# Performance work log

Measured on AMD Instinct MI355X. Metric: run time of the kernel, lower is better.

Reference implementation:

```python
import jax, jax.numpy as jnp
import numpy as np

N = 30000   # total nodes
E = 240000  # edges
B = 64      # graphs / proteins
H = 10      # GATv2 heads
C = 78      # per-head out dim (= xd_features)
D = H * C   # 780
SEQ = 1000
EMB = 128
LH = 64     # LSTM hidden per direction


def _lstm_dir(xs, Wih, Whh, bih, bhh, reverse):
    # xs: [T, Bn, EMB]; PyTorch gate order i,f,g,o
    Bn = xs.shape[1]
    h0 = jnp.zeros((Bn, LH), xs.dtype)
    def step(carry, xt):
        h, c = carry
        z = xt @ Wih.T + h @ Whh.T + bih + bhh
        i, f, g, o = jnp.split(z, 4, axis=-1)
        c = jax.nn.sigmoid(f) * c + jax.nn.sigmoid(i) * jnp.tanh(g)
        h = jax.nn.sigmoid(o) * jnp.tanh(c)
        return (h, c), h
    _, hs = jax.lax.scan(step, (h0, h0), xs, reverse=reverse)
    return hs


def setup_inputs() -> dict:
    k = jax.random.key(0)
    nxt = lambda i: jax.random.fold_in(k, i)
    s = 0.05
    d = {}
    d['x'] = jax.random.normal(nxt(0), (N, C), jnp.float32)
    d['edge_index'] = jax.random.randint(nxt(1), (2, E), 0, N)
    d['batch'] = jnp.sort(jax.random.randint(nxt(2), (N,), 0, B))
    d['target'] = jax.random.randint(nxt(3), (B, SEQ), 0, 26)
    # GATv2Conv params (share_weights=False)
    d['Wl'] = jax.random.normal(nxt(4), (C, D), jnp.float32) * s
    d['Wr'] = jax.random.normal(nxt(5), (C, D), jnp.float32) * s
    d['att'] = jax.random.normal(nxt(6), (H, C), jnp.float32) * s
    d['gat_b'] = jnp.zeros((D,), jnp.float32)
    # GCNConv params
    d['gcn_w'] = jax.random.normal(nxt(7), (D, D), jnp.float32) * s
    d['gcn_b'] = jnp.zeros((D,), jnp.float32)
    # protein branch
    d['emb'] = jax.random.normal(nxt(8), (26, EMB), jnp.float32) * s
    for tag, base in (('f', 9), ('b', 13)):
        d['Wih_' + tag] = jax.random.normal(nxt(base), (4 * LH, EMB), jnp.float32) * s
        d['Whh_' + tag] = jax.random.normal(nxt(base + 1), (4 * LH, LH), jnp.float32) * s
        d['bih_' + tag] = jnp.zeros((4 * LH,), jnp.float32)
        d['bhh_' + tag] = jnp.zeros((4 * LH,), jnp.float32)
    d['conv_w'] = jax.random.normal(nxt(17), (32, SEQ, 8), jnp.float32) * s
    d['conv_b'] = jnp.zeros((32,), jnp.float32)
    d['fcp_w'] = jax.random.normal(nxt(18), (32 * 121, 128), jnp.float32) * s
    d['fcp_b'] = jnp.zeros((128,), jnp.float32)
    # combined MLP (actual concat dim = 2*780 + 128 = 1688)
    d['fc1_w'] = jax.random.normal(nxt(19), (1688, 1024), jnp.float32) * s
    d['fc1_b'] = jnp.zeros((1024,), jnp.float32)
    d['fc2_w'] = jax.random.normal(nxt(20), (1024, 512), jnp.float32) * s
    d['fc2_b'] = jnp.zeros((512,), jnp.float32)
    d['out_w'] = jax.random.normal(nxt(21), (512, 1), jnp.float32) * s
    d['out_b'] = jnp.zeros((1,), jnp.float32)
    return d


def reference(x, edge_index, batch, target, Wl, Wr, att, gat_b, gcn_w, gcn_b,
              emb, Wih_f, Whh_f, bih_f, bhh_f, Wih_b, Whh_b, bih_b, bhh_b,
              conv_w, conv_b, fcp_w, fcp_b, fc1_w, fc1_b, fc2_w, fc2_b,
              out_w, out_b):
    # ---- graph branch (eval mode: dropout off) ----
    loops = jnp.arange(N)
    src = jnp.concatenate([edge_index[0], loops])  # self loops (PyG default)
    dst = jnp.concatenate([edge_index[1], loops])

    # GATv2Conv
    xl = (x @ Wl).reshape(N, H, C)
    xr = (x @ Wr).reshape(N, H, C)
    e = jax.nn.leaky_relu(xl[src] + xr[dst], 0.2)       # [E+N, H, C]
    logit = jnp.einsum('ehc,hc->eh', e, att)            # [E+N, H]
    m = jax.ops.segment_max(logit, dst, num_segments=N)
    ex = jnp.exp(logit - m[dst])
    den = jax.ops.segment_sum(ex, dst, num_segments=N)
    alpha = ex / den[dst]
    h = jax.ops.segment_sum(alpha[:, :, None] * xl[src], dst, num_segments=N)
    h = jax.nn.elu(h.reshape(N, D) + gat_b)

    # GCNConv with symmetric normalization
    hw = h @ gcn_w
    deg = jax.ops.segment_sum(jnp.ones_like(src, jnp.float32), dst, num_segments=N)
    dinv = jnp.where(deg > 0, jax.lax.rsqrt(jnp.maximum(deg, 1e-12)), 0.0)
    norm = dinv[src] * dinv[dst]
    g = jax.ops.segment_sum(norm[:, None] * hw[src], dst, num_segments=N) + gcn_b
    g = jax.nn.relu(g)

    # global max + mean pooling per graph
    gmax = jax.ops.segment_max(g, batch, num_segments=B)
    cnt = jax.ops.segment_sum(jnp.ones((N,), jnp.float32), batch, num_segments=B)
    gmean = jax.ops.segment_sum(g, batch, num_segments=B) / jnp.maximum(cnt, 1.0)[:, None]
    graph_feat = jnp.concatenate([gmax, gmean], axis=1)  # [B, 1560]

    # ---- protein branch ----
    et = emb[target]                                     # [B, SEQ, EMB]
    # nn.LSTM default batch_first=False: time axis is axis 0 (=B), batch axis is SEQ
    hf = _lstm_dir(et, Wih_f, Whh_f, bih_f, bhh_f, reverse=False)
    hb = _lstm_dir(et, Wih_b, Whh_b, bih_b, bhh_b, reverse=True)
    hcat = jnp.concatenate([hf, hb], axis=-1)            # [B, SEQ, 128]
    conv = jax.lax.conv_general_dilated(hcat, conv_w, (1,), 'VALID',
                                        dimension_numbers=('NCH', 'OIH', 'NCH'))
    conv = conv + conv_b[None, :, None]                  # [B, 32, 121]
    prot = conv.reshape(B, 32 * 121) @ fcp_w + fcp_b     # [B, 128]

    # ---- combined head ----
    comb = jnp.concatenate([graph_feat, prot], axis=1)   # [B, 1688]
    h1 = jax.nn.relu(comb @ fc1_w + fc1_b)
    h2 = jax.nn.relu(h1 @ fc2_w + fc2_b)
    return h2 @ out_w + out_b                            # [B, 1]
```

## Files before the change

kernel.cpp:

```cpp
#include <hip/hip_runtime.h>
#include <hip/hip_bf16.h>
#include <math.h>

static constexpr int NN   = 30000;
static constexpr int EE   = 240000;
static constexpr int ET   = EE + NN;
static constexpr int BB   = 64;
static constexpr int HH   = 10;
static constexpr int CC   = 78;
static constexpr int CCP  = 80;
static constexpr int DD   = HH * CC;
static constexpr int DDP  = HH * CCP;
static constexpr int NNP  = 30080;
static constexpr int KXP  = 96;
static constexpr int NBP  = 896;
static constexpr int SEQ  = 1000;
static constexpr int EMB  = 128;
static constexpr int LH   = 64;
static constexpr int COMBD = 2 * DD + 128;
static constexpr int PCHUNK = 64;

typedef __attribute__((ext_vector_type(8))) short short8;
typedef __attribute__((ext_vector_type(4))) float f32x4;

__device__ __forceinline__ float bf2f(unsigned short u) {
    return __uint_as_float(((unsigned int)u) << 16);
}
__device__ __forceinline__ float bflo(unsigned int u) {
    return __uint_as_float(u << 16);
}
__device__ __forceinline__ float bfhi(unsigned int u) {
    return __uint_as_float(u & 0xffff0000u);
}
__device__ __forceinline__ unsigned int pack2bf(float x, float y) {
    __hip_bfloat16 bx = __float2bfloat16(x), by = __float2bfloat16(y);
    unsigned short ux = *reinterpret_cast<unsigned short*>(&bx);
    unsigned short uy = *reinterpret_cast<unsigned short*>(&by);
    return (unsigned int)ux | ((unsigned int)uy << 16);
}
__device__ __forceinline__ float fast_sigmoid(float x) {
    return __builtin_amdgcn_rcpf(1.f + __expf(-x));
}
__device__ __forceinline__ float fast_tanh(float x) {
    float e = __expf(2.f * x);
    return 1.f - 2.f * __builtin_amdgcn_rcpf(e + 1.f);
}
__device__ __forceinline__ void glds16(const unsigned short* g, unsigned short* l) {
    __builtin_amdgcn_global_load_lds(
        (const __attribute__((address_space(1))) unsigned int*)g,
        (__attribute__((address_space(3))) unsigned int*)l, 16, 0, 0);
}

template <int PADHEAD>
__global__ __launch_bounds__(256) void gemm_glds(const __hip_bfloat16* __restrict__ A,
                                                 const __hip_bfloat16* __restrict__ Bt,
                                                 __hip_bfloat16* __restrict__ C,
                                                 int M, int N, int Kp, int ldc) {
    __shared__ unsigned short As[128 * 32];
    __shared__ unsigned short Bs[128 * 32];
    const int tid  = threadIdx.x;
    const int lane = tid & 63, wid = tid >> 6;
    const int wr = wid >> 1, wc = wid & 1;
    const int l15 = lane & 15, l4 = lane >> 4;
    int l = blockIdx.y * gridDim.x + blockIdx.x;
    {
        int nwg = gridDim.x * gridDim.y;
        int q = nwg >> 3, r = nwg & 7;
        int xcd = l & 7, idx = l >> 3;
        l = (xcd < r) ? (xcd * (q + 1) + idx) : (r * (q + 1) + (xcd - r) * q + idx);
    }
    const int bm = (l / gridDim.x) * 128;
    const int bn = (l % gridDim.x) * 128;
    const unsigned short* Au = (const unsigned short*)A;
    const unsigned short* Bu = (const unsigned short*)Bt;
    const int lrow = lane >> 2, lseg = (lane & 3) * 8;

    f32x4 acc[4][4];
#pragma unroll
    for (int m = 0; m < 4; ++m)
#pragma unroll
        for (int n = 0; n < 4; ++n) acc[m][n] = (f32x4){0.f, 0.f, 0.f, 0.f};

    for (int k0 = 0; k0 < Kp; k0 += 32) {
#pragma unroll
        for (int c = 0; c < 2; ++c) {
            int rbase = wid * 32 + c * 16;
            glds16(Au + (size_t)(bm + rbase + lrow) * Kp + k0 + lseg, &As[rbase * 32]);
            glds16(Bu + (size_t)(bn + rbase + lrow) * Kp + k0 + lseg, &Bs[rbase * 32]);
        }
        __syncthreads();
        short8 a[4], b[4];
#pragma unroll
        for (int m = 0; m < 4; ++m)
            a[m] = *reinterpret_cast<const short8*>(&As[(wr * 64 + m * 16 + l15) * 32 + l4 * 8]);
#pragma unroll
        for (int n = 0; n < 4; ++n)
            b[n] = *reinterpret_cast<const short8*>(&Bs[(wc * 64 + n * 16 + l15) * 32 + l4 * 8]);
#pragma unroll
        for (int m = 0; m < 4; ++m)
#pragma unroll
            for (int n = 0; n < 4; ++n)
                acc[m][n] = __builtin_amdgcn_mfma_f32_16x16x32_bf16(a[m], b[n], acc[m][n], 0, 0, 0);
        __syncthreads();
    }
#pragma unroll
    for (int m = 0; m < 4; ++m)
#pragma unroll
        for (int n = 0; n < 4; ++n)
#pragma unroll
            for (int r = 0; r < 4; ++r) {
                int row = bm + wr * 64 + m * 16 + l4 * 4 + r;
                int col = bn + wc * 64 + n * 16 + l15;
                if (row < M && col < N) {
                    int pc = PADHEAD ? ((col / CC) * CCP + (col % CC)) : col;
                    C[(size_t)row * ldc + pc] = __float2bfloat16(acc[m][n][r]);
                }
            }
}

template <int OBF, int PADHEAD>
__global__ __launch_bounds__(256) void gemm_bf16_mfma(const __hip_bfloat16* __restrict__ A,
                                                      const __hip_bfloat16* __restrict__ Bt,
                                                      void* __restrict__ Cv,
                                                      int M, int N, int K, int ldc) {
    constexpr int LDS_S = 40;
    __shared__ unsigned short As[128 * LDS_S];
    __shared__ unsigned short Bs[128 * LDS_S];
    const int tid  = threadIdx.x;
    const int lane = tid & 63, wid = tid >> 6;
    const int wr = wid >> 1, wc = wid & 1;
    const int l15 = lane & 15, l4 = lane >> 4;
    int l = blockIdx.y * gridDim.x + blockIdx.x;
    {
        int nwg = gridDim.x * gridDim.y;
        int q = nwg >> 3, r = nwg & 7;
        int xcd = l & 7, idx = l >> 3;
        l = (xcd < r) ? (xcd * (q + 1) + idx) : (r * (q + 1) + (xcd - r) * q + idx);
    }
    const int bm = (l / gridDim.x) * 128;
    const int bn = (l % gridDim.x) * 128;
    const int tr = tid >> 2, tc = (tid & 3) * 8;

    const unsigned short* Au = (const unsigned short*)A;
    const unsigned short* Bu = (const unsigned short*)Bt;

    f32x4 acc[4][4];
#pragma unroll
    for (int m = 0; m < 4; ++m)
#pragma unroll
        for (int n = 0; n < 4; ++n) acc[m][n] = (f32x4){0.f, 0.f, 0.f, 0.f};

    for (int k0 = 0; k0 < K; k0 += 32) {
#pragma unroll
        for (int half = 0; half < 2; ++half) {
            int row = tr + half * 64;
            {
                int grow = bm + row;
                short8 sv;
                if (grow < M && k0 + tc + 8 <= K) {
                    const unsigned int* p = (const unsigned int*)(Au + (size_t)grow * K + k0 + tc);
#pragma unroll
                    for (int j = 0; j < 4; ++j) {
                        unsigned int u = p[j];
                        sv[2 * j]     = (short)(u & 0xffffu);
                        sv[2 * j + 1] = (short)(u >> 16);
                    }
                } else {
#pragma unroll
                    for (int j = 0; j < 8; ++j) {
                        int gk = k0 + tc + j;
                        sv[j] = (grow < M && gk < K) ? (short)Au[(size_t)grow * K + gk] : (short)0;
                    }
                }
                *reinterpret_cast<short8*>(&As[row * LDS_S + tc]) = sv;
            }
            {
                int grow = bn + row;
                short8 sv;
                if (grow < N && k0 + tc + 8 <= K) {
                    const unsigned int* p = (const unsigned int*)(Bu + (size_t)grow * K + k0 + tc);
#pragma unroll
                    for (int j = 0; j < 4; ++j) {
                        unsigned int u = p[j];
                        sv[2 * j]     = (short)(u & 0xffffu);
                        sv[2 * j + 1] = (short)(u >> 16);
                    }
                } else {
#pragma unroll
                    for (int j = 0; j < 8; ++j) {
                        int gk = k0 + tc + j;
                        sv[j] = (grow < N && gk < K) ? (short)Bu[(size_t)grow * K + gk] : (short)0;
                    }
                }
                *reinterpret_cast<short8*>(&Bs[row * LDS_S + tc]) = sv;
            }
        }
        __syncthreads();
        short8 a[4], b[4];
#pragma unroll
        for (int m = 0; m < 4; ++m)
            a[m] = *reinterpret_cast<const short8*>(&As[(wr * 64 + m * 16 + l15) * LDS_S + l4 * 8]);
#pragma unroll
        for (int n = 0; n < 4; ++n)
            b[n] = *reinterpret_cast<const short8*>(&Bs[(wc * 64 + n * 16 + l15) * LDS_S + l4 * 8]);
#pragma unroll
        for (int m = 0; m < 4; ++m)
#pragma unroll
            for (int n = 0; n < 4; ++n)
                acc[m][n] = __builtin_amdgcn_mfma_f32_16x16x32_bf16(a[m], b[n], acc[m][n], 0, 0, 0);
        __syncthreads();
    }
#pragma unroll
    for (int m = 0; m < 4; ++m)
#pragma unroll
        for (int n = 0; n < 4; ++n)
#pragma unroll
            for (int r = 0; r < 4; ++r) {
                int row = bm + wr * 64 + m * 16 + l4 * 4 + r;
                int col = bn + wc * 64 + n * 16 + l15;
                if (row < M && col < N) {
                    int pc = PADHEAD ? ((col / CC) * CCP + (col % CC)) : col;
                    if (OBF)
                        ((__hip_bfloat16*)Cv)[(size_t)row * ldc + pc] = __float2bfloat16(acc[m][n][r]);
                    else
                        ((float*)Cv)[(size_t)row * ldc + pc] = acc[m][n][r];
                }
            }
}

__global__ void pad_x(const float* __restrict__ x, __hip_bfloat16* __restrict__ xp) {
    int idx = blockIdx.x * blockDim.x + threadIdx.x;
    if (idx >= NNP * KXP) return;
    int r = idx / KXP, c = idx % KXP;
    float v = (r < NN && c < CC) ? x[(size_t)r * CC + c] : 0.f;
    xp[idx] = __float2bfloat16(v);
}

__global__ void pad_wT(const float* __restrict__ w, __hip_bfloat16* __restrict__ wt) {
    int idx = blockIdx.x * blockDim.x + threadIdx.x;
    if (idx >= NBP * KXP) return;
    int n = idx / KXP, k = idx % KXP;
    float v = (n < DD && k < CC) ? w[(size_t)k * DD + n] : 0.f;
    wt[idx] = __float2bfloat16(v);
}

__global__ void pad_gcwT(const float* __restrict__ w, __hip_bfloat16* __restrict__ wt) {
    int idx = blockIdx.x * blockDim.x + threadIdx.x;
    if (idx >= NBP * DDP) return;
    int n = idx / DDP, kp = idx % DDP;
    int kc = kp % CCP;
    int k = (kp / CCP) * CC + kc;
    float v = (n < DD && kc < CC) ? w[(size_t)k * DD + n] : 0.f;
    wt[idx] = __float2bfloat16(v);
}

__global__ void transpose_f32(const float* __restrict__ in, float* __restrict__ out,
                              int Kdim, int Ndim) {
    int idx = blockIdx.x * blockDim.x + threadIdx.x;
    if (idx >= Kdim * Ndim) return;
    int n = idx / Kdim, k = idx % Kdim;
    out[idx] = in[(size_t)k * Ndim + n];
}

__global__ void pad_att(const float* __restrict__ att, float* __restrict__ att_p) {
    int idx = blockIdx.x * blockDim.x + threadIdx.x;
    if (idx >= HH * CCP) return;
    int h = idx / CCP, c = idx % CCP;
    att_p[idx] = (c < CC) ? att[h * CC + c] : 0.f;
}

__global__ void zero_pads(unsigned int* __restrict__ a, unsigned int* __restrict__ b) {
    int idx = blockIdx.x * blockDim.x + threadIdx.x;
    if (idx >= NN * HH) return;
    int n = idx / HH, h = idx % HH;
    size_t p = ((size_t)n * DDP + h * CCP + CC) >> 1;
    a[p] = 0u;
    b[p] = 0u;
}

template <int ACT>
__global__ __launch_bounds__(256) void gemm_skinny(const float* __restrict__ A,
                                                   const float* __restrict__ Bt,
                                                   const float* __restrict__ bias,
                                                   float* __restrict__ C,
                                                   int M, int N, int K, int ldc) {
    int oidx = blockIdx.x * 4 + (threadIdx.x >> 6);
    int lane = threadIdx.x & 63;
    if (oidx >= M * N) return;
    int row = oidx / N, col = oidx % N;
    const float4* a = (const float4*)(A + (size_t)row * K);
    const float4* b = (const float4*)(Bt + (size_t)col * K);
    int K4 = K >> 2;
    float s = 0.f;
    for (int i = lane; i < K4; i += 64) {
        float4 x = a[i], y = b[i];
        s += x.x * y.x + x.y * y.y + x.z * y.z + x.w * y.w;
    }
#pragma unroll
    for (int off = 32; off; off >>= 1) s += __shfl_xor(s, off);
    if (lane == 0) {
        s += bias[col];
        if (ACT == 1) s = fmaxf(s, 0.f);
        C[(size_t)row * ldc + col] = s;
    }
}

__global__ void deg_count(const int* __restrict__ ei, int* __restrict__ deg) {
    int e = blockIdx.x * blockDim.x + threadIdx.x;
    if (e >= ET) return;
    int d = (e < EE) ? ei[EE + e] : (e - EE);
    atomicAdd(&deg[d], 1);
}

__global__ __launch_bounds__(1024) void scan_kernel(const int* __restrict__ deg,
                                                    int* __restrict__ offs) {
    __shared__ int lds[1024];
    int tid = threadIdx.x;
    const int chunk = (NN + 1023) / 1024;
    int base = tid * chunk;
    int s = 0;
    for (int i = 0; i < chunk; ++i) {
        int idx = base + i;
        if (idx < NN) s += deg[idx];
    }
    lds[tid] = s;
    __syncthreads();
    for (int d = 1; d < 1024; d <<= 1) {
        int v = (tid >= d) ? lds[tid - d] : 0;
        __syncthreads();
        lds[tid] += v;
        __syncthreads();
    }
    int run = (tid == 0) ? 0 : lds[tid - 1];
    for (int i = 0; i < chunk; ++i) {
        int idx = base + i;
        if (idx < NN) { offs[idx] = run; run += deg[idx]; }
    }
    if (tid == 1023) offs[NN] = lds[1023];
}

__global__ void csr_fill(const int* __restrict__ ei, const int* __restrict__ offs,
                         int* __restrict__ cursor, int* __restrict__ csr_src,
                         int* __restrict__ csr_dst) {
    int e = blockIdx.x * blockDim.x + threadIdx.x;
    if (e >= ET) return;
    int s = (e < EE) ? ei[e] : (e - EE);
    int d = (e < EE) ? ei[EE + e] : (e - EE);
    int pos = atomicAdd(&cursor[d], 1);
    int slot = offs[d] + pos;
    csr_src[slot] = s;
    csr_dst[slot] = d;
}

__global__ void dinv_kernel(const int* __restrict__ deg, float* __restrict__ dinv) {
    int n = blockIdx.x * blockDim.x + threadIdx.x;
    if (n >= NN) return;
    float dg = (float)deg[n];
    dinv[n] = (dg > 0.f) ? 1.f / sqrtf(dg) : 0.f;
}

__device__ __forceinline__ float dot2lr(unsigned int a, unsigned int b, float w0, float w1) {
    float v0 = bflo(a) + bflo(b);
    float v1 = bfhi(a) + bfhi(b);
    v0 = (v0 > 0.f) ? v0 : 0.2f * v0;
    v1 = (v1 > 0.f) ? v1 : 0.2f * v1;
    return w0 * v0 + w1 * v1;
}

__global__ void gat_logits(const unsigned short* __restrict__ xl,
                           const unsigned short* __restrict__ xr,
                           const float* __restrict__ att_p, const int* __restrict__ csr_src,
                           const int* __restrict__ csr_dst, float* __restrict__ logit) {
    int idx = blockIdx.x * blockDim.x + threadIdx.x;
    if (idx >= ET * HH) return;
    int i = idx / HH, h = idx % HH;
    int s = csr_src[i], d = csr_dst[i];
    const uint4* pl = (const uint4*)(xl + (size_t)s * DDP + h * CCP);
    const uint4* pr = (const uint4*)(xr + (size_t)d * DDP + h * CCP);
    const float* pa = att_p + h * CCP;
    float acc = 0.f;
#pragma unroll
    for (int q = 0; q < CCP / 8; ++q) {
        uint4 a = pl[q], b = pr[q];
        const float* p8 = pa + q * 8;
        acc += dot2lr(a.x, b.x, p8[0], p8[1]);
        acc += dot2lr(a.y, b.y, p8[2], p8[3]);
        acc += dot2lr(a.z, b.z, p8[4], p8[5]);
        acc += dot2lr(a.w, b.w, p8[6], p8[7]);
    }
    logit[idx] = acc;
}

__global__ void gat_softmax(const int* __restrict__ offs, float* __restrict__ logit) {
    int idx = blockIdx.x * blockDim.x + threadIdx.x;
    if (idx >= NN * HH) return;
    int n = idx / HH, h = idx % HH;
    int i0 = offs[n], i1 = offs[n + 1];
    float m = -1e30f;
    for (int i = i0; i < i1; ++i) m = fmaxf(m, logit[i * HH + h]);
    float den = 0.f;
    for (int i = i0; i < i1; ++i) {
        float e = __expf(logit[i * HH + h] - m);
        logit[i * HH + h] = e;
        den += e;
    }
    float inv = __builtin_amdgcn_rcpf(den);
    for (int i = i0; i < i1; ++i) logit[i * HH + h] *= inv;
}

__global__ __launch_bounds__(256) void gat_aggregate(const int* __restrict__ offs,
                                                     const int* __restrict__ csr_src,
                                                     const float* __restrict__ alpha,
                                                     const unsigned int* __restrict__ xl,
                                                     const float* __restrict__ gat_b,
                                                     unsigned int* __restrict__ hout) {
    int n = blockIdx.x;
    int tid = threadIdx.x;
    int i0 = offs[n], i1 = offs[n + 1];
    const int U = DDP / 2;
    int u0 = tid, u1 = tid + 256;
    bool v1 = (u1 < U);
    int h0 = u0 / (CCP / 2), h1 = v1 ? u1 / (CCP / 2) : 0;
    float lo0 = 0.f, hi0 = 0.f, lo1 = 0.f, hi1 = 0.f;
    for (int i = i0; i < i1; ++i) {
        const unsigned int* row = xl + (size_t)csr_src[i] * U;
        const float* al = alpha + (size_t)i * HH;
        unsigned int w0 = row[u0];
        float p0 = al[h0];
        lo0 += p0 * bflo(w0);
        hi0 += p0 * bfhi(w0);
        if (v1) {
            unsigned int w1 = row[u1];
            float p1 = al[h1];
            lo1 += p1 * bflo(w1);
            hi1 += p1 * bfhi(w1);
        }
    }
    unsigned int ov0 = 0u, ov1 = 0u;
    int m0 = u0 % (CCP / 2);
    if (m0 != (CCP / 2 - 1)) {
        int d = h0 * CC + 2 * m0;
        float x = lo0 + gat_b[d];     x = (x > 0.f) ? x : __expf(x) - 1.f;
        float y = hi0 + gat_b[d + 1]; y = (y > 0.f) ? y : __expf(y) - 1.f;
        ov0 = pack2bf(x, y);
    }
    hout[(size_t)n * U + u0] = ov0;
    if (v1) {
        int m1 = u1 % (CCP / 2);
        if (m1 != (CCP / 2 - 1)) {
            int d = h1 * CC + 2 * m1;
            float x = lo1 + gat_b[d];     x = (x > 0.f) ? x : __expf(x) - 1.f;
            float y = hi1 + gat_b[d + 1]; y = (y > 0.f) ? y : __expf(y) - 1.f;
            ov1 = pack2bf(x, y);
        }
        hout[(size_t)n * U + u1] = ov1;
    }
}

__global__ __launch_bounds__(256) void gcn_aggregate(const int* __restrict__ offs,
                                                     const int* __restrict__ csr_src,
                                                     const float* __restrict__ dinv,
                                                     const unsigned int* __restrict__ hw,
                                                     const float* __restrict__ gcn_b,
                                                     unsigned int* __restrict__ g) {
    int n = blockIdx.x;
    int tid = threadIdx.x;
    float din = dinv[n];
    int i0 = offs[n], i1 = offs[n + 1];
    const int U = DDP / 2;
    int u0 = tid, u1 = tid + 256;
    bool v1 = (u1 < U);
    float lo0 = 0.f, hi0 = 0.f, lo1 = 0.f, hi1 = 0.f;
    for (int i = i0; i < i1; ++i) {
        int s = csr_src[i];
        float w = dinv[s] * din;
        const unsigned int* row = hw + (size_t)s * U;
        unsigned int w0 = row[u0];
        lo0 += w * bflo(w0);
        hi0 += w * bfhi(w0);
        if (v1) {
            unsigned int w1 = row[u1];
            lo1 += w * bflo(w1);
            hi1 += w * bfhi(w1);
        }
    }
    int m0 = u0 % (CCP / 2);
    if (m0 != (CCP / 2 - 1)) {
        int d = (u0 / (CCP / 2)) * CC + 2 * m0;
        float x = fmaxf(lo0 + gcn_b[d], 0.f);
        float y = fmaxf(hi0 + gcn_b[d + 1], 0.f);
        g[(size_t)n * U + u0] = pack2bf(x, y);
    }
    if (v1) {
        int m1 = u1 % (CCP / 2);
        if (m1 != (CCP / 2 - 1)) {
            int d = (u1 / (CCP / 2)) * CC + 2 * m1;
            float x = fmaxf(lo1 + gcn_b[d], 0.f);
            float y = fmaxf(hi1 + gcn_b[d + 1], 0.f);
            g[(size_t)n * U + u1] = pack2bf(x, y);
        }
    }
}

__global__ void graph_ranges(const int* __restrict__ batch, int* __restrict__ gstart,
                             int* __restrict__ gend) {
    int n = blockIdx.x * blockDim.x + threadIdx.x;
    if (n >= NN) return;
    int b = batch[n];
    if (n == 0 || batch[n - 1] != b) gstart[b] = n;
    if (n == NN - 1 || batch[n + 1] != b) gend[b] = n + 1;
}

__global__ __launch_bounds__(256) void pool_partial(const unsigned int* __restrict__ g,
                                                    const int* __restrict__ batch,
                                                    float* __restrict__ pmax,
                                                    float* __restrict__ psum) {
    int chunk0 = blockIdx.x * PCHUNK;
    int tid = threadIdx.x;
    __shared__ int bsh[PCHUNK];
    for (int i = tid; i < PCHUNK; i += 256) {
        int n = chunk0 + i;
        bsh[i] = (n < NN) ? batch[n] : -1;
    }
    __syncthreads();
    const int U = DDP / 2;
    int u0 = tid, u1 = tid + 256;
    bool v1 = (u1 < U);
    float mA = 0.f, mB = 0.f, mC = 0.f, mD = 0.f;
    float sA = 0.f, sB = 0.f, sC = 0.f, sD = 0.f;
    int curb = bsh[0];
    auto flush = [&](int b) {
        if (b >= 0) {
            int m0 = u0 % (CCP / 2);
            if (m0 != (CCP / 2 - 1)) {
                int d = (u0 / (CCP / 2)) * CC + 2 * m0;
                atomicMax((unsigned int*)&pmax[(size_t)b * DD + d], __float_as_uint(mA));
                atomicAdd(&psum[(size_t)b * DD + d], sA);
                atomicMax((unsigned int*)&pmax[(size_t)b * DD + d + 1], __float_as_uint(mB));
                atomicAdd(&psum[(size_t)b * DD + d + 1], sB);
            }
            if (v1) {
                int m1 = u1 % (CCP / 2);
                if (m1 != (CCP / 2 - 1)) {
                    int d = (u1 / (CCP / 2)) * CC + 2 * m1;
                    atomicMax((unsigned int*)&pmax[(size_t)b * DD + d], __float_as_uint(mC));
                    atomicAdd(&psum[(size_t)b * DD + d], sC);
                    atomicMax((unsigned int*)&pmax[(size_t)b * DD + d + 1], __float_as_uint(mD));
                    atomicAdd(&psum[(size_t)b * DD + d + 1], sD);
                }
            }
        }
        mA = mB = mC = mD = 0.f;
        sA = sB = sC = sD = 0.f;
    };
    for (int i = 0; i < PCHUNK; ++i) {
        int n = chunk0 + i;
        if (n >= NN) break;
        int b = bsh[i];
        if (b != curb) { flush(curb); curb = b; }
        const unsigned int* row = g + (size_t)n * U;
        unsigned int w0 = row[u0];
        float x = bflo(w0), y = bfhi(w0);
        mA = fmaxf(mA, x); sA += x;
        mB = fmaxf(mB, y); sB += y;
        if (v1) {
            unsigned int w1 = row[u1];
            float z = bflo(w1), t = bfhi(w1);
            mC = fmaxf(mC, z); sC += z;
            mD = fmaxf(mD, t); sD += t;
        }
    }
    flush(curb);
}

__global__ void pool_finalize(const float* __restrict__ pmax, const float* __restrict__ psum,
                              const int* __restrict__ gstart, const int* __restrict__ gend,
                              float* __restrict__ comb) {
    int idx = blockIdx.x * blockDim.x + threadIdx.x;
    if (idx >= BB * DD) return;
    int b = idx / DD, d = idx % DD;
    float cnt = fmaxf((float)(gend[b] - gstart[b]), 1.f);
    comb[(size_t)b * COMBD + d] = pmax[idx];
    comb[(size_t)b * COMBD + DD + d] = psum[idx] / cnt;
}

__global__ void proj26_kernel(const float* __restrict__ emb,
                              const float* __restrict__ Wih_f, const float* __restrict__ bih_f,
                              const float* __restrict__ bhh_f,
                              const float* __restrict__ Wih_b, const float* __restrict__ bih_b,
                              const float* __restrict__ bhh_b, float* __restrict__ proj) {
    int dir = blockIdx.x, row = blockIdx.y, j = threadIdx.x;
    const float* W = dir ? Wih_b : Wih_f;
    const float* b1 = dir ? bih_b : bih_f;
    const float* b2 = dir ? bhh_b : bhh_f;
    float acc = b1[j] + b2[j];
    const float* e = emb + row * EMB;
    const float* w = W + j * EMB;
    for (int k = 0; k < EMB; ++k) acc += e[k] * w[k];
    proj[(dir * 26 + row) * 256 + j] = acc;
}

__global__ __launch_bounds__(256) void lstm_kernel(const int* __restrict__ target,
                                                   const float* __restrict__ proj26,
                                                   const float* __restrict__ Whh_f,
                                                   const float* __restrict__ Whh_b,
                                                   float* __restrict__ hcat) {
    int n = blockIdx.x;
    int dir = blockIdx.y;
    int tid = threadIdx.x;
    const float* Whh = dir ? Whh_b : Whh_f;
    const float* proj = proj26 + dir * 26 * 256;
    const int gate = tid >> 6;
    float w[LH];
#pragma unroll
    for (int u4 = 0; u4 < LH / 4; ++u4) {
        float4 v = *reinterpret_cast<const float4*>(Whh + tid * LH + u4 * 4);
        w[u4 * 4 + 0] = v.x; w[u4 * 4 + 1] = v.y;
        w[u4 * 4 + 2] = v.z; w[u4 * 4 + 3] = v.w;
    }
    __shared__ float h_lds[LH];
    __shared__ float z_lds[256];
    float c_reg = 0.f;
    if (tid < LH) h_lds[tid] = 0.f;
    __syncthreads();
    for (int s = 0; s < BB; ++s) {
        int t = dir ? (BB - 1 - s) : s;
        int tgt = target[t * SEQ + n];
        float a0 = 0.f, a1 = 0.f, a2 = 0.f, a3 = 0.f;
#pragma unroll
        for (int u = 0; u < LH; u += 4) {
            a0 += w[u] * h_lds[u];
            a1 += w[u + 1] * h_lds[u + 1];
            a2 += w[u + 2] * h_lds[u + 2];
            a3 += w[u + 3] * h_lds[u + 3];
        }
        float z = proj[tgt * 256 + tid] + a0 + a1 + a2 + a3;
        z_lds[tid] = (gate == 2) ? fast_tanh(z) : fast_sigmoid(z);
        __syncthreads();
        if (tid < LH) {
            float ig = z_lds[tid];
            float fg = z_lds[LH + tid];
            float gg = z_lds[2 * LH + tid];
            float og = z_lds[3 * LH + tid];
            float c = fg * c_reg + ig * gg;
            float h = og * fast_tanh(c);
            c_reg = c;
            h_lds[tid] = h;
            hcat[((size_t)t * SEQ + n) * 128 + dir * LH + tid] = h;
        }
        __syncthreads();
    }
}

__global__ __launch_bounds__(256) void transpose_hcat(const float* __restrict__ hcat,
                                                      unsigned short* __restrict__ hcatT) {
    int b = blockIdx.z;
    int i0 = blockIdx.y * 32;
    int h0 = blockIdx.x * 32;
    int th = threadIdx.x & 31;
    int ti = threadIdx.x >> 5;
    __shared__ float t[32][33];
#pragma unroll
    for (int r = 0; r < 4; ++r) {
        int i = i0 + ti + r * 8;
        if (i < SEQ) t[ti + r * 8][th] = hcat[((size_t)b * SEQ + i) * 128 + h0 + th];
    }
    __syncthreads();
#pragma unroll
    for (int r = 0; r < 4; ++r) {
        int h = h0 + ti + r * 8;
        int i = i0 + th;
        if (i < SEQ) {
            unsigned int u = __float_as_uint(t[th][ti + r * 8]);
            unsigned int lsb = (u >> 16) & 1u;
            u += 0x7fffu + lsb;
            hcatT[((size_t)b * 128 + h) * SEQ + i] = (unsigned short)(u >> 16);
        }
    }
}

__global__ void reshape_convw(const float* __restrict__ conv_w, __hip_bfloat16* __restrict__ wT) {
    int idx = blockIdx.x * blockDim.x + threadIdx.x;
    if (idx >= 256 * SEQ) return;
    int np = idx / SEQ, i = idx % SEQ;
    int o = np >> 3, k = np & 7;
    wT[idx] = __float2bfloat16(conv_w[((size_t)o * SEQ + i) * 8 + k]);
}

__global__ void conv_finalize(const float* __restrict__ T, const float* __restrict__ conv_b,
                              float* __restrict__ convout) {
    int idx = blockIdx.x * blockDim.x + threadIdx.x;
    if (idx >= BB * 32 * 121) return;
    int p = idx % 121;
    int o = (idx / 121) % 32;
    int b = idx / (121 * 32);
    float acc = conv_b[o];
#pragma unroll
    for (int k = 0; k < 8; ++k)
        acc += T[(size_t)(b * 128 + p + k) * 256 + o * 8 + k];
    convout[(size_t)b * 3872 + o * 121 + p] = acc;
}

extern "C" void kernel_launch(void* const* d_in, const int* in_sizes, int n_in,
                              void* d_out, int out_size, void* d_ws, size_t ws_size,
                              hipStream_t stream) {
    const float* x      = (const float*)d_in[0];
    const int*   ei     = (const int*)d_in[1];
    const int*   batch  = (const int*)d_in[2];
    const int*   target = (const int*)d_in[3];
    const float* Wl     = (const float*)d_in[4];
    const float* Wr     = (const float*)d_in[5];
    const float* att    = (const float*)d_in[6];
    const float* gat_b  = (const float*)d_in[7];
    const float* gcn_w  = (const float*)d_in[8];
    const float* gcn_b  = (const float*)d_in[9];
    const float* emb    = (const float*)d_in[10];
    const float* Wih_f  = (const float*)d_in[11];
    const float* Whh_f  = (const float*)d_in[12];
    const float* bih_f  = (const float*)d_in[13];
    const float* bhh_f  = (const float*)d_in[14];
    const float* Wih_b  = (const float*)d_in[15];
    const float* Whh_b  = (const float*)d_in[16];
    const float* bih_b  = (const float*)d_in[17];
    const float* bhh_b  = (const float*)d_in[18];
    const float* conv_w = (const float*)d_in[19];
    const float* conv_b = (const float*)d_in[20];
    const float* fcp_w  = (const float*)d_in[21];
    const float* fcp_b  = (const float*)d_in[22];
    const float* fc1_w  = (const float*)d_in[23];
    const float* fc1_b  = (const float*)d_in[24];
    const float* fc2_w  = (const float*)d_in[25];
    const float* fc2_b  = (const float*)d_in[26];
    const float* out_w  = (const float*)d_in[27];
    const float* out_b  = (const float*)d_in[28];
    float* out = (float*)d_out;
    (void)n_in; (void)in_sizes; (void)out_size;

    char* ws = (char*)d_ws;
    size_t o = 0;
    auto alloc = [&](size_t bytes) {
        char* p = ws + o;
        o = (o + bytes + 255) & ~(size_t)255;
        return p;
    };
    constexpr size_t HALF = (size_t)NN * DDP * 2;
    char* region = (char*)alloc(2 * HALF);
    __hip_bfloat16* xl_bf = (__hip_bfloat16*)region;
    __hip_bfloat16* xr_bf = (__hip_bfloat16*)(region + HALF);
    __hip_bfloat16* hw_bf = (__hip_bfloat16*)region;
    __hip_bfloat16* g_bf  = (__hip_bfloat16*)(region + HALF);
    char* rp = region;
    auto palloc = [&](size_t bytes) {
        char* p = rp;
        rp += (bytes + 255) & ~(size_t)255;
        return p;
    };
    float* hcat    = (float*)palloc((size_t)BB * SEQ * 128 * 4);
    float* proj26  = (float*)palloc(2 * 26 * 256 * 4);
    float* convout = (float*)palloc((size_t)BB * 3872 * 4);
    __hip_bfloat16* wT = (__hip_bfloat16*)palloc((size_t)256 * SEQ * 2);
    unsigned short* hcatT = (unsigned short*)palloc((size_t)BB * 128 * SEQ * 2);
    float* T = (float*)palloc((size_t)BB * 128 * 256 * 4);
    __hip_bfloat16* h_bf  = (__hip_bfloat16*)alloc((size_t)NNP * DDP * 2);
    __hip_bfloat16* x_bf  = (__hip_bfloat16*)alloc((size_t)NNP * KXP * 2);
    __hip_bfloat16* wl_t  = (__hip_bfloat16*)alloc((size_t)NBP * KXP * 2);
    __hip_bfloat16* wr_t  = (__hip_bfloat16*)alloc((size_t)NBP * KXP * 2);
    __hip_bfloat16* gcw_t = (__hip_bfloat16*)alloc((size_t)NBP * DDP * 2);
    float* att_p  = (float*)alloc((size_t)HH * CCP * 4);
    float* fcp_wt = (float*)alloc((size_t)3872 * 128 * 4);
    float* fc1_wt = (float*)alloc((size_t)COMBD * 1024 * 4);
    float* fc2_wt = (float*)alloc((size_t)1024 * 512 * 4);
    float* out_wt = (float*)alloc((size_t)512 * 4);
    float* logit    = (float*)alloc((size_t)ET * HH * 4);
    int*   csr_src  = (int*)alloc((size_t)ET * 4);
    int*   csr_dst  = (int*)alloc((size_t)ET * 4);
    int*   deg      = (int*)alloc((size_t)NN * 4);
    int*   cursor   = (int*)alloc((size_t)NN * 4);
    int*   offs     = (int*)alloc((size_t)(NN + 1) * 4);
    float* dinv     = (float*)alloc((size_t)NN * 4);
    int*   gstart   = (int*)alloc(64 * 4);
    int*   gend     = (int*)alloc(64 * 4);
    float* pmax     = (float*)alloc((size_t)BB * DD * 4);
    float* psum     = (float*)alloc((size_t)BB * DD * 4);
    float* comb     = (float*)alloc((size_t)BB * COMBD * 4);
    float* h1       = (float*)alloc((size_t)BB * 1024 * 4);
    float* h2       = (float*)alloc((size_t)BB * 512 * 4);
    if (o > ws_size) return;

    hipMemsetAsync(deg, 0, (size_t)NN * 4, stream);
    hipMemsetAsync(cursor, 0, (size_t)NN * 4, stream);
    hipMemsetAsync(gstart, 0, 64 * 4, stream);
    hipMemsetAsync(gend, 0, 64 * 4, stream);
    hipMemsetAsync(pmax, 0, (size_t)BB * DD * 4, stream);
    hipMemsetAsync(psum, 0, (size_t)BB * DD * 4, stream);

    {
        dim3 grid(2, 26);
        proj26_kernel<<<grid, 256, 0, stream>>>(emb, Wih_f, bih_f, bhh_f, Wih_b, bih_b, bhh_b, proj26);
    }
    {
        dim3 grid(SEQ, 2);
        lstm_kernel<<<grid, 256, 0, stream>>>(target, proj26, Whh_f, Whh_b, hcat);
    }
    {
        dim3 grid(4, 32, BB);
        transpose_hcat<<<grid, 256, 0, stream>>>(hcat, hcatT);
    }
    reshape_convw<<<(256 * SEQ + 255) / 256, 256, 0, stream>>>(conv_w, wT);
    {
        dim3 grid(2, 64);
        gemm_bf16_mfma<0, 0><<<grid, 256, 0, stream>>>((const __hip_bfloat16*)hcatT, wT, T,
                                                       BB * 128, 256, SEQ, 256);
    }
    conv_finalize<<<(BB * 32 * 121 + 255) / 256, 256, 0, stream>>>(T, conv_b, convout);
    transpose_f32<<<(3872 * 128 + 255) / 256, 256, 0, stream>>>(fcp_w, fcp_wt, 3872, 128);
    gemm_skinny<0><<<(BB * 128 + 3) / 4, 256, 0, stream>>>(convout, fcp_wt, fcp_b,
                                                           comb + 2 * DD, BB, 128, 3872, COMBD);

    pad_x<<<(NNP * KXP + 255) / 256, 256, 0, stream>>>(x, x_bf);
    pad_wT<<<(NBP * KXP + 255) / 256, 256, 0, stream>>>(Wl, wl_t);
    pad_wT<<<(NBP * KXP + 255) / 256, 256, 0, stream>>>(Wr, wr_t);
    pad_gcwT<<<(NBP * DDP + 255) / 256, 256, 0, stream>>>(gcn_w, gcw_t);
    pad_att<<<(HH * CCP + 255) / 256, 256, 0, stream>>>(att, att_p);
    transpose_f32<<<(COMBD * 1024 + 255) / 256, 256, 0, stream>>>(fc1_w, fc1_wt, COMBD, 1024);
    transpose_f32<<<(1024 * 512 + 255) / 256, 256, 0, stream>>>(fc2_w, fc2_wt, 1024, 512);
    transpose_f32<<<(512 + 255) / 256, 256, 0, stream>>>(out_w, out_wt, 512, 1);

    dim3 ggrid((DD + 127) / 128, NNP / 128);
    gemm_glds<1><<<ggrid, 256, 0, stream>>>(x_bf, wl_t, xl_bf, NN, DD, KXP, DDP);
    gemm_glds<1><<<ggrid, 256, 0, stream>>>(x_bf, wr_t, xr_bf, NN, DD, KXP, DDP);
    zero_pads<<<(NN * HH + 255) / 256, 256, 0, stream>>>((unsigned int*)xl_bf, (unsigned int*)xr_bf);
    deg_count<<<(ET + 255) / 256, 256, 0, stream>>>(ei, deg);
    scan_kernel<<<1, 1024, 0, stream>>>(deg, offs);
    csr_fill<<<(ET + 255) / 256, 256, 0, stream>>>(ei, offs, cursor, csr_src, csr_dst);
    dinv_kernel<<<(NN + 255) / 256, 256, 0, stream>>>(deg, dinv);
    gat_logits<<<(ET * HH + 255) / 256, 256, 0, stream>>>((const unsigned short*)xl_bf,
                                                          (const unsigned short*)xr_bf,
                                                          att_p, csr_src, csr_dst, logit);
    gat_softmax<<<(NN * HH + 255) / 256, 256, 0, stream>>>(offs, logit);
    gat_aggregate<<<NN, 256, 0, stream>>>(offs, csr_src, logit,
                                          (const unsigned int*)xl_bf, gat_b,
                                          (unsigned int*)h_bf);
    {
        dim3 g2((DD + 127) / 128, NNP / 128);
        gemm_glds<1><<<g2, 256, 0, stream>>>(h_bf, gcw_t, hw_bf, NN, DD, DDP, DDP);
    }
    gcn_aggregate<<<NN, 256, 0, stream>>>(offs, csr_src, dinv,
                                          (const unsigned int*)hw_bf, gcn_b,
                                          (unsigned int*)g_bf);
    graph_ranges<<<(NN + 255) / 256, 256, 0, stream>>>(batch, gstart, gend);
    pool_partial<<<(NN + PCHUNK - 1) / PCHUNK, 256, 0, stream>>>((const unsigned int*)g_bf,
                                                                 batch, pmax, psum);
    pool_finalize<<<(BB * DD + 255) / 256, 256, 0, stream>>>(pmax, psum, gstart, gend, comb);

    gemm_skinny<1><<<(BB * 1024 + 3) / 4, 256, 0, stream>>>(comb, fc1_wt, fc1_b, h1,
                                                            BB, 1024, COMBD, 1024);
    gemm_skinny<1><<<(BB * 512 + 3) / 4, 256, 0, stream>>>(h1, fc2_wt, fc2_b, h2,
                                                           BB, 512, 1024, 512);
    gemm_skinny<0><<<(BB + 3) / 4, 256, 0, stream>>>(h2, out_wt, out_b, out,
                                                     BB, 1, 512, 1);
}
```

Before: 870.9 us.

## Store node features in head-major slices and head-major logits

Node feature matrices (xl, xr, hw, g) are now stored as per-head slices of [nodes x 80] instead of row-major [nodes x 800], and attention logits are stored head-major. GAT logits use a 2D grid with one head per block row. The aim is better cache locality in the gathers, since each head's slice of a source row is compact and neighbouring threads in the edge-parallel kernels touch the same head's data. In exchange, the per-node aggregation kernels now read from ten separate slices per node, which scatters their memory accesses across distant addresses.

Result: no change. 876.9 us (+0.7%).

```diff
diff --git a/kernel.cpp b/kernel.cpp
--- a/kernel.cpp
+++ b/kernel.cpp
@@ -19,13 +19,12 @@
 static constexpr int LH   = 64;
 static constexpr int COMBD = 2 * DD + 128;
 static constexpr int PCHUNK = 64;
+static constexpr int USL  = CCP / 2;
+static constexpr size_t SLICE_U = (size_t)NNP * USL;
 
 typedef __attribute__((ext_vector_type(8))) short short8;
 typedef __attribute__((ext_vector_type(4))) float f32x4;
 
-__device__ __forceinline__ float bf2f(unsigned short u) {
-    return __uint_as_float(((unsigned int)u) << 16);
-}
 __device__ __forceinline__ float bflo(unsigned int u) {
     return __uint_as_float(u << 16);
 }
@@ -51,11 +50,10 @@
         (__attribute__((address_space(3))) unsigned int*)l, 16, 0, 0);
 }
 
-template <int PADHEAD>
-__global__ __launch_bounds__(256) void gemm_glds(const __hip_bfloat16* __restrict__ A,
-                                                 const __hip_bfloat16* __restrict__ Bt,
-                                                 __hip_bfloat16* __restrict__ C,
-                                                 int M, int N, int Kp, int ldc) {
+__global__ __launch_bounds__(256) void gemm_glds_sl(const __hip_bfloat16* __restrict__ A,
+                                                    const __hip_bfloat16* __restrict__ Bt,
+                                                    __hip_bfloat16* __restrict__ C,
+                                                    int M, int N, int Kp) {
     __shared__ unsigned short As[128 * 32];
     __shared__ unsigned short Bs[128 * 32];
     const int tid  = threadIdx.x;
@@ -112,16 +110,16 @@
                 int row = bm + wr * 64 + m * 16 + l4 * 4 + r;
                 int col = bn + wc * 64 + n * 16 + l15;
                 if (row < M && col < N) {
-                    int pc = PADHEAD ? ((col / CC) * CCP + (col % CC)) : col;
-                    C[(size_t)row * ldc + pc] = __float2bfloat16(acc[m][n][r]);
+                    int sl = col / CC, c = col % CC;
+                    C[(size_t)sl * NNP * CCP + (size_t)row * CCP + c] =
+                        __float2bfloat16(acc[m][n][r]);
                 }
             }
 }
 
-template <int OBF, int PADHEAD>
 __global__ __launch_bounds__(256) void gemm_bf16_mfma(const __hip_bfloat16* __restrict__ A,
                                                       const __hip_bfloat16* __restrict__ Bt,
-                                                      void* __restrict__ Cv,
+                                                      float* __restrict__ C,
                                                       int M, int N, int K, int ldc) {
     constexpr int LDS_S = 40;
     __shared__ unsigned short As[128 * LDS_S];
@@ -218,13 +216,8 @@
             for (int r = 0; r < 4; ++r) {
                 int row = bm + wr * 64 + m * 16 + l4 * 4 + r;
                 int col = bn + wc * 64 + n * 16 + l15;
-                if (row < M && col < N) {
-                    int pc = PADHEAD ? ((col / CC) * CCP + (col % CC)) : col;
-                    if (OBF)
-                        ((__hip_bfloat16*)Cv)[(size_t)row * ldc + pc] = __float2bfloat16(acc[m][n][r]);
-                    else
-                        ((float*)Cv)[(size_t)row * ldc + pc] = acc[m][n][r];
-                }
+                if (row < M && col < N)
+                    C[(size_t)row * ldc + col] = acc[m][n][r];
             }
 }
 
@@ -273,7 +266,7 @@
     int idx = blockIdx.x * blockDim.x + threadIdx.x;
     if (idx >= NN * HH) return;
     int n = idx / HH, h = idx % HH;
-    size_t p = ((size_t)n * DDP + h * CCP + CC) >> 1;
+    size_t p = (size_t)h * SLICE_U + (size_t)n * USL + (USL - 1);
     a[p] = 0u;
     b[p] = 0u;
 }
@@ -367,16 +360,16 @@
     return w0 * v0 + w1 * v1;
 }
 
-__global__ void gat_logits(const unsigned short* __restrict__ xl,
-                           const unsigned short* __restrict__ xr,
+__global__ void gat_logits(const unsigned short* __restrict__ xl_sl,
+                           const unsigned short* __restrict__ xr_sl,
                            const float* __restrict__ att_p, const int* __restrict__ csr_src,
-                           const int* __restrict__ csr_dst, float* __restrict__ logit) {
-    int idx = blockIdx.x * blockDim.x + threadIdx.x;
-    if (idx >= ET * HH) return;
-    int i = idx / HH, h = idx % HH;
+                           const int* __restrict__ csr_dst, float* __restrict__ logit_hm) {
+    int i = blockIdx.x * blockDim.x + threadIdx.x;
+    int h = blockIdx.y;
+    if (i >= ET) return;
     int s = csr_src[i], d = csr_dst[i];
-    const uint4* pl = (const uint4*)(xl + (size_t)s * DDP + h * CCP);
-    const uint4* pr = (const uint4*)(xr + (size_t)d * DDP + h * CCP);
+    const uint4* pl = (const uint4*)(xl_sl + (size_t)h * NNP * CCP + (size_t)s * CCP);
+    const uint4* pr = (const uint4*)(xr_sl + (size_t)h * NNP * CCP + (size_t)d * CCP);
     const float* pa = att_p + h * CCP;
     float acc = 0.f;
 #pragma unroll
@@ -388,30 +381,31 @@
         acc += dot2lr(a.z, b.z, p8[4], p8[5]);
         acc += dot2lr(a.w, b.w, p8[6], p8[7]);
     }
-    logit[idx] = acc;
-}
-
-__global__ void gat_softmax(const int* __restrict__ offs, float* __restrict__ logit) {
+    logit_hm[(size_t)h * ET + i] = acc;
+}
+
+__global__ void gat_softmax(const int* __restrict__ offs, float* __restrict__ logit_hm) {
     int idx = blockIdx.x * blockDim.x + threadIdx.x;
     if (idx >= NN * HH) return;
     int n = idx / HH, h = idx % HH;
     int i0 = offs[n], i1 = offs[n + 1];
+    float* lg = logit_hm + (size_t)h * ET;
     float m = -1e30f;
-    for (int i = i0; i < i1; ++i) m = fmaxf(m, logit[i * HH + h]);
+    for (int i = i0; i < i1; ++i) m = fmaxf(m, lg[i]);
     float den = 0.f;
     for (int i = i0; i < i1; ++i) {
-        float e = __expf(logit[i * HH + h] - m);
-        logit[i * HH + h] = e;
+        float e = __expf(lg[i] - m);
+        lg[i] = e;
         den += e;
     }
     float inv = __builtin_amdgcn_rcpf(den);
-    for (int i = i0; i < i1; ++i) logit[i * HH + h] *= inv;
+    for (int i = i0; i < i1; ++i) lg[i] *= inv;
 }
 
 __global__ __launch_bounds__(256) void gat_aggregate(const int* __restrict__ offs,
                                                      const int* __restrict__ csr_src,
-                                                     const float* __restrict__ alpha,
-                                                     const unsigned int* __restrict__ xl,
+                                                     const float* __restrict__ alpha_hm,
+                                                     const unsigned int* __restrict__ xl_sl,
                                                      const float* __restrict__ gat_b,
                                                      unsigned int* __restrict__ hout) {
     int n = blockIdx.x;
@@ -420,35 +414,37 @@
     const int U = DDP / 2;
     int u0 = tid, u1 = tid + 256;
     bool v1 = (u1 < U);
-    int h0 = u0 / (CCP / 2), h1 = v1 ? u1 / (CCP / 2) : 0;
+    int h0 = u0 / USL, c0 = u0 % USL;
+    int h1 = v1 ? u1 / USL : 0, c1 = v1 ? u1 % USL : 0;
+    const unsigned int* s0 = xl_sl + (size_t)h0 * SLICE_U + c0;
+    const unsigned int* s1 = xl_sl + (size_t)h1 * SLICE_U + c1;
+    const float* a0p = alpha_hm + (size_t)h0 * ET;
+    const float* a1p = alpha_hm + (size_t)h1 * ET;
     float lo0 = 0.f, hi0 = 0.f, lo1 = 0.f, hi1 = 0.f;
     for (int i = i0; i < i1; ++i) {
-        const unsigned int* row = xl + (size_t)csr_src[i] * U;
-        const float* al = alpha + (size_t)i * HH;
-        unsigned int w0 = row[u0];
-        float p0 = al[h0];
+        int src = csr_src[i];
+        unsigned int w0 = s0[(size_t)src * USL];
+        float p0 = a0p[i];
         lo0 += p0 * bflo(w0);
         hi0 += p0 * bfhi(w0);
         if (v1) {
-            unsigned int w1 = row[u1];
-            float p1 = al[h1];
+            unsigned int w1 = s1[(size_t)src * USL];
+            float p1 = a1p[i];
             lo1 += p1 * bflo(w1);
             hi1 += p1 * bfhi(w1);
         }
     }
     unsigned int ov0 = 0u, ov1 = 0u;
-    int m0 = u0 % (CCP / 2);
-    if (m0 != (CCP / 2 - 1)) {
-        int d = h0 * CC + 2 * m0;
+    if (c0 != USL - 1) {
+        int d = h0 * CC + 2 * c0;
         float x = lo0 + gat_b[d];     x = (x > 0.f) ? x : __expf(x) - 1.f;
         float y = hi0 + gat_b[d + 1]; y = (y > 0.f) ? y : __expf(y) - 1.f;
         ov0 = pack2bf(x, y);
     }
     hout[(size_t)n * U + u0] = ov0;
     if (v1) {
-        int m1 = u1 % (CCP / 2);
-        if (m1 != (CCP / 2 - 1)) {
-            int d = h1 * CC + 2 * m1;
+        if (c1 != USL - 1) {
+            int d = h1 * CC + 2 * c1;
             float x = lo1 + gat_b[d];     x = (x > 0.f) ? x : __expf(x) - 1.f;
             float y = hi1 + gat_b[d + 1]; y = (y > 0.f) ? y : __expf(y) - 1.f;
             ov1 = pack2bf(x, y);
@@ -460,9 +456,9 @@
 __global__ __launch_bounds__(256) void gcn_aggregate(const int* __restrict__ offs,
                                                      const int* __restrict__ csr_src,
                                                      const float* __restrict__ dinv,
-                                                     const unsigned int* __restrict__ hw,
+                                                     const unsigned int* __restrict__ hw_sl,
                                                      const float* __restrict__ gcn_b,
-                                                     unsigned int* __restrict__ g) {
+                                                     unsigned int* __restrict__ g_sl) {
     int n = blockIdx.x;
     int tid = threadIdx.x;
     float din = dinv[n];
@@ -470,35 +466,34 @@
     const int U = DDP / 2;
     int u0 = tid, u1 = tid + 256;
     bool v1 = (u1 < U);
+    int h0 = u0 / USL, c0 = u0 % USL;
+    int h1 = v1 ? u1 / USL : 0, c1 = v1 ? u1 % USL : 0;
+    const unsigned int* s0 = hw_sl + (size_t)h0 * SLICE_U + c0;
+    const unsigned int* s1 = hw_sl + (size_t)h1 * SLICE_U + c1;
     float lo0 = 0.f, hi0 = 0.f, lo1 = 0.f, hi1 = 0.f;
     for (int i = i0; i < i1; ++i) {
-        int s = csr_src[i];
-        float w = dinv[s] * din;
-        const unsigned int* row = hw + (size_t)s * U;
-        unsigned int w0 = row[u0];
+        int src = csr_src[i];
+        float w = dinv[src] * din;
+        unsigned int w0 = s0[(size_t)src * USL];
         lo0 += w * bflo(w0);
         hi0 += w * bfhi(w0);
         if (v1) {
-            unsigned int w1 = row[u1];
+            unsigned int w1 = s1[(size_t)src * USL];
             lo1 += w * bflo(w1);
             hi1 += w * bfhi(w1);
         }
     }
-    int m0 = u0 % (CCP / 2);
-    if (m0 != (CCP / 2 - 1)) {
-        int d = (u0 / (CCP / 2)) * CC + 2 * m0;
+    if (c0 != USL - 1) {
+        int d = h0 * CC + 2 * c0;
         float x = fmaxf(lo0 + gcn_b[d], 0.f);
         float y = fmaxf(hi0 + gcn_b[d + 1], 0.f);
-        g[(size_t)n * U + u0] = pack2bf(x, y);
-    }
-    if (v1) {
-        int m1 = u1 % (CCP / 2);
-        if (m1 != (CCP / 2 - 1)) {
-            int d = (u1 / (CCP / 2)) * CC + 2 * m1;
-            float x = fmaxf(lo1 + gcn_b[d], 0.f);
-            float y = fmaxf(hi1 + gcn_b[d + 1], 0.f);
-            g[(size_t)n * U + u1] = pack2bf(x, y);
-        }
+        g_sl[(size_t)h0 * SLICE_U + (size_t)n * USL + c0] = pack2bf(x, y);
+    }
+    if (v1 && c1 != USL - 1) {
+        int d = h1 * CC + 2 * c1;
+        float x = fmaxf(lo1 + gcn_b[d], 0.f);
+        float y = fmaxf(hi1 + gcn_b[d + 1], 0.f);
+        g_sl[(size_t)h1 * SLICE_U + (size_t)n * USL + c1] = pack2bf(x, y);
     }
 }
 
@@ -511,7 +506,7 @@
     if (n == NN - 1 || batch[n + 1] != b) gend[b] = n + 1;
 }
 
-__global__ __launch_bounds__(256) void pool_partial(const unsigned int* __restrict__ g,
+__global__ __launch_bounds__(256) void pool_partial(const unsigned int* __restrict__ g_sl,
                                                     const int* __restrict__ batch,
                                                     float* __restrict__ pmax,
                                                     float* __restrict__ psum) {
@@ -526,28 +521,28 @@
     const int U = DDP / 2;
     int u0 = tid, u1 = tid + 256;
     bool v1 = (u1 < U);
+    int h0 = u0 / USL, c0 = u0 % USL;
+    int h1 = v1 ? u1 / USL : 0, c1 = v1 ? u1 % USL : 0;
+    const unsigned int* s0 = g_sl + (size_t)h0 * SLICE_U + c0;
+    const unsigned int* s1 = g_sl + (size_t)h1 * SLICE_U + c1;
     float mA = 0.f, mB = 0.f, mC = 0.f, mD = 0.f;
     float sA = 0.f, sB = 0.f, sC = 0.f, sD = 0.f;
     int curb = bsh[0];
     auto flush = [&](int b) {
         if (b >= 0) {
-            int m0 = u0 % (CCP / 2);
-            if (m0 != (CCP / 2 - 1)) {
-                int d = (u0 / (CCP / 2)) * CC + 2 * m0;
+            if (c0 != USL - 1) {
+                int d = h0 * CC + 2 * c0;
                 atomicMax((unsigned int*)&pmax[(size_t)b * DD + d], __float_as_uint(mA));
                 atomicAdd(&psum[(size_t)b * DD + d], sA);
                 atomicMax((unsigned int*)&pmax[(size_t)b * DD + d + 1], __float_as_uint(mB));
                 atomicAdd(&psum[(size_t)b * DD + d + 1], sB);
             }
-            if (v1) {
-                int m1 = u1 % (CCP / 2);
-                if (m1 != (CCP / 2 - 1)) {
-                    int d = (u1 / (CCP / 2)) * CC + 2 * m1;
-                    atomicMax((unsigned int*)&pmax[(size_t)b * DD + d], __float_as_uint(mC));
-                    atomicAdd(&psum[(size_t)b * DD + d], sC);
-                    atomicMax((unsigned int*)&pmax[(size_t)b * DD + d + 1], __float_as_uint(mD));
-                    atomicAdd(&psum[(size_t)b * DD + d + 1], sD);
-                }
+            if (v1 && c1 != USL - 1) {
+                int d = h1 * CC + 2 * c1;
+                atomicMax((unsigned int*)&pmax[(size_t)b * DD + d], __float_as_uint(mC));
+                atomicAdd(&psum[(size_t)b * DD + d], sC);
+                atomicMax((unsigned int*)&pmax[(size_t)b * DD + d + 1], __float_as_uint(mD));
+                atomicAdd(&psum[(size_t)b * DD + d + 1], sD);
             }
         }
         mA = mB = mC = mD = 0.f;
@@ -558,13 +553,12 @@
         if (n >= NN) break;
         int b = bsh[i];
         if (b != curb) { flush(curb); curb = b; }
-        const unsigned int* row = g + (size_t)n * U;
-        unsigned int w0 = row[u0];
+        unsigned int w0 = s0[(size_t)n * USL];
         float x = bflo(w0), y = bfhi(w0);
         mA = fmaxf(mA, x); sA += x;
         mB = fmaxf(mB, y); sB += y;
         if (v1) {
-            unsigned int w1 = row[u1];
+            unsigned int w1 = s1[(size_t)n * USL];
             float z = bflo(w1), t = bfhi(w1);
             mC = fmaxf(mC, z); sC += z;
             mD = fmaxf(mD, t); sD += t;
@@ -743,12 +737,12 @@
         o = (o + bytes + 255) & ~(size_t)255;
         return p;
     };
-    constexpr size_t HALF = (size_t)NN * DDP * 2;
+    constexpr size_t HALF = (size_t)HH * NNP * CCP * 2;
     char* region = (char*)alloc(2 * HALF);
-    __hip_bfloat16* xl_bf = (__hip_bfloat16*)region;
-    __hip_bfloat16* xr_bf = (__hip_bfloat16*)(region + HALF);
-    __hip_bfloat16* hw_bf = (__hip_bfloat16*)region;
-    __hip_bfloat16* g_bf  = (__hip_bfloat16*)(region + HALF);
+    __hip_bfloat16* xl_sl = (__hip_bfloat16*)region;
+    __hip_bfloat16* xr_sl = (__hip_bfloat16*)(region + HALF);
+    __hip_bfloat16* hw_sl = (__hip_bfloat16*)region;
+    __hip_bfloat16* g_sl  = (__hip_bfloat16*)(region + HALF);
     char* rp = region;
     auto palloc = [&](size_t bytes) {
         char* p = rp;
@@ -809,8 +803,8 @@
     reshape_convw<<<(256 * SEQ + 255) / 256, 256, 0, stream>>>(conv_w, wT);
     {
         dim3 grid(2, 64);
-        gemm_bf16_mfma<0, 0><<<grid, 256, 0, stream>>>((const __hip_bfloat16*)hcatT, wT, T,
-                                                       BB * 128, 256, SEQ, 256);
+        gemm_bf16_mfma<<<grid, 256, 0, stream>>>((const __hip_bfloat16*)hcatT, wT, T,
+                                                 BB * 128, 256, SEQ, 256);
     }
     conv_finalize<<<(BB * 32 * 121 + 255) / 256, 256, 0, stream>>>(T, conv_b, convout);
     transpose_f32<<<(3872 * 128 + 255) / 256, 256, 0, stream>>>(fcp_w, fcp_wt, 3872, 128);
@@ -827,29 +821,32 @@
     transpose_f32<<<(512 + 255) / 256, 256, 0, stream>>>(out_w, out_wt, 512, 1);
 
     dim3 ggrid((DD + 127) / 128, NNP / 128);
-    gemm_glds<1><<<ggrid, 256, 0, stream>>>(x_bf, wl_t, xl_bf, NN, DD, KXP, DDP);
-    gemm_glds<1><<<ggrid, 256, 0, stream>>>(x_bf, wr_t, xr_bf, NN, DD, KXP, DDP);
-    zero_pads<<<(NN * HH + 255) / 256, 256, 0, stream>>>((unsigned int*)xl_bf, (unsigned int*)xr_bf);
+    gemm_glds_sl<<<ggrid, 256, 0, stream>>>(x_bf, wl_t, xl_sl, NN, DD, KXP);
+    gemm_glds_sl<<<ggrid, 256, 0, stream>>>(x_bf, wr_t, xr_sl, NN, DD, KXP);
+    zero_pads<<<(NN * HH + 255) / 256, 256, 0, stream>>>((unsigned int*)xl_sl, (unsigned int*)xr_sl);
     deg_count<<<(ET + 255) / 256, 256, 0, stream>>>(ei, deg);
     scan_kernel<<<1, 1024, 0, stream>>>(deg, offs);
     csr_fill<<<(ET + 255) / 256, 256, 0, stream>>>(ei, offs, cursor, csr_src, csr_dst);
     dinv_kernel<<<(NN + 255) / 256, 256, 0, stream>>>(deg, dinv);
-    gat_logits<<<(ET * HH + 255) / 256, 256, 0, stream>>>((const unsigned short*)xl_bf,
-                                                          (const unsigned short*)xr_bf,
-                                                          att_p, csr_src, csr_dst, logit);
+    {
+        dim3 grid((ET + 255) / 256, HH);
+        gat_logits<<<grid, 256, 0, stream>>>((const unsigned short*)xl_sl,
+                                             (const unsigned short*)xr_sl,
+                                             att_p, csr_src, csr_dst, logit);
+    }
     gat_softmax<<<(NN * HH + 255) / 256, 256, 0, stream>>>(offs, logit);
     gat_aggregate<<<NN, 256, 0, stream>>>(offs, csr_src, logit,
-                                          (const unsigned int*)xl_bf, gat_b,
+                                          (const unsigned int*)xl_sl, gat_b,
                                           (unsigned int*)h_bf);
     {
         dim3 g2((DD + 127) / 128, NNP / 128);
-        gemm_glds<1><<<g2, 256, 0, stream>>>(h_bf, gcw_t, hw_bf, NN, DD, DDP, DDP);
+        gemm_glds_sl<<<g2, 256, 0, stream>>>(h_bf, gcw_t, hw_sl, NN, DD, DDP);
     }
     gcn_aggregate<<<NN, 256, 0, stream>>>(offs, csr_src, dinv,
-                                          (const unsigned int*)hw_bf, gcn_b,
-                                          (unsigned int*)g_bf);
+                                          (const unsigned int*)hw_sl, gcn_b,
+                                          (unsigned int*)g_sl);
     graph_ranges<<<(NN + 255) / 256, 256, 0, stream>>>(batch, gstart, gend);
-    pool_partial<<<(NN + PCHUNK - 1) / PCHUNK, 256, 0, stream>>>((const unsigned int*)g_bf,
+    pool_partial<<<(NN + PCHUNK - 1) / PCHUNK, 256, 0, stream>>>((const unsigned int*)g_sl,
                                                                  batch, pmax, psum);
     pool_finalize<<<(BB * DD + 255) / 256, 256, 0, stream>>>(pmax, psum, gstart, gend, comb);
 
```
